# Performance work log

Measured on AMD Instinct MI355X. Metric: run time of the kernel, lower is better.

The kernel has to match this reference:

```python
import jax, jax.numpy as jnp
import numpy as np
from jax import lax

B, C, H = 16384, 512, 1024
IN = C + 4  # context + prev_delta(2) + heading(2)
LN_EPS = 1e-5


def _layernorm(x, g, b):
    mu = x.mean(-1, keepdims=True)
    var = ((x - mu) ** 2).mean(-1, keepdims=True)
    return (x - mu) * lax.rsqrt(var + LN_EPS) * g + b


def setup_inputs() -> dict:
    key = jax.random.key(0)
    ks = jax.random.split(key, 16)
    s = lambda fan_in: 1.0 / np.sqrt(fan_in)
    return {
        "context": jax.random.normal(ks[0], (B, C), jnp.float32),
        "last_pos": jax.random.normal(ks[1], (B, 2), jnp.float32),
        "last_delta": jax.random.normal(ks[2], (B, 2), jnp.float32) * 0.1,
        "Wh": jax.random.normal(ks[3], (H, C), jnp.float32) * s(C),
        "bh": jnp.zeros((H,), jnp.float32),
        "Wc": jax.random.normal(ks[4], (H, C), jnp.float32) * s(C),
        "bc": jnp.zeros((H,), jnp.float32),
        "W_ih": jax.random.normal(ks[5], (4 * H, IN), jnp.float32) * s(H),
        "b_ih": jax.random.normal(ks[6], (4 * H,), jnp.float32) * s(H),
        "W_hh": jax.random.normal(ks[7], (4 * H, H), jnp.float32) * s(H),
        "b_hh": jax.random.normal(ks[8], (4 * H,), jnp.float32) * s(H),
        "ln_g": jnp.ones((H,), jnp.float32),
        "ln_b": jnp.zeros((H,), jnp.float32),
        "W1": jax.random.normal(ks[9], (H, H), jnp.float32) * s(H),
        "b1": jnp.zeros((H,), jnp.float32),
        "W2": jax.random.normal(ks[10], (2, H), jnp.float32) * s(H),
        "b2": jnp.zeros((2,), jnp.float32),
        "pred_len": 60,
    }


def reference(context, last_pos, last_delta, Wh, bh, Wc, bc, W_ih, b_ih, W_hh, b_hh,
              ln_g, ln_b, W1, b1, W2, b2, pred_len):
    hidden = jnp.tanh(context @ Wh.T + bh)
    cell = jnp.tanh(context @ Wc.T + bc)
    # context part of LSTM input gates is constant across steps: precompute
    gates_ctx = context @ W_ih[:, :C].T + b_ih  # [B, 4H]
    W_extra = W_ih[:, C:]  # [4H, 4]

    def step(carry, _):
        h, c, pos, pd = carry
        heading = pd / jnp.maximum(jnp.linalg.norm(pd, axis=-1, keepdims=True), 1e-6)
        extra = jnp.concatenate([pd, heading], axis=-1)  # [B,4]
        gates = gates_ctx + extra @ W_extra.T + h @ W_hh.T + b_hh
        i, f, g, o = jnp.split(gates, 4, axis=-1)
        c = jax.nn.sigmoid(f) * c + jax.nn.sigmoid(i) * jnp.tanh(g)
        h = jax.nn.sigmoid(o) * jnp.tanh(c)
        y = _layernorm(h, ln_g, ln_b)  # dropout is identity in eval
        y = jax.nn.gelu(y @ W1.T + b1, approximate=False)
        delta = y @ W2.T + b2  # [B,2]
        pos = pos + delta
        return (h, c, pos, delta), pos

    _, outs = lax.scan(step, (hidden, cell, last_pos, last_delta), None, length=pred_len)
    return jnp.swapaxes(outs, 0, 1)  # [B, pred_len, 2]
```

## Files before the change

### kernel.cpp

```cpp
#include <hip/hip_runtime.h>
#include <math.h>

constexpr int BATCH = 16384;
constexpr int CDIM  = 512;
constexpr int HDIM  = 1024;
constexpr int GDIM  = 4096;
constexpr int TSTEP = 60;
constexpr float LOSC  = 2048.0f;
constexpr float ILOSC = 1.0f / 2048.0f;

typedef _Float16 half_t;
typedef _Float16 halfx8 __attribute__((ext_vector_type(8)));
typedef _Float16 halfx4 __attribute__((ext_vector_type(4)));
typedef float    f32x4  __attribute__((ext_vector_type(4)));
typedef int      i32x4  __attribute__((ext_vector_type(4)));
typedef signed char i8_t;

__device__ __forceinline__ void async_cp16(const void* g, void* l) {
  __builtin_amdgcn_global_load_lds((__attribute__((address_space(1))) void*)g,
                                   (__attribute__((address_space(3))) void*)l,
                                   16, 0, 0);
}

__device__ __forceinline__ half_t hi16(float x) { return (half_t)x; }
__device__ __forceinline__ half_t lo16(float x) {
  return (half_t)((x - (float)((half_t)x)) * LOSC);
}
__device__ __forceinline__ int clamp8(int v) {
  return v > 127 ? 127 : (v < -127 ? -127 : v);
}
__device__ __forceinline__ float sigf(float x) { return 1.0f / (1.0f + expf(-x)); }
__device__ __forceinline__ float geluf(float v) {
  return 0.5f * v * (1.0f + erff(v * 0.70710678118f));
}

__device__ __forceinline__ void swizzle_tiles(int& mt, int& nt) {
  const int gx = gridDim.x, gy = gridDim.y;
  if (gy & 7) { mt = blockIdx.x; nt = blockIdx.y; return; }
  const int lin = blockIdx.y * gx + blockIdx.x;
  const int xcd = lin & 7;
  const int slot = lin >> 3;
  const int npx = gy >> 3;
  nt = xcd * npx + (slot % npx);
  mt = slot / npx;
}

__device__ __forceinline__ void kstep(f32x4 (&acc)[4][4],
    const half_t* __restrict__ A, size_t lda, int krel,
    const half_t* __restrict__ W, size_t ldw, int kw,
    half_t* sA, half_t* sB, int bm0, int bn0) {
  const int tid  = threadIdx.x;
  const int lane = tid & 63;
  const int wave = tid >> 6;
  const int wm = wave >> 1, wn = wave & 1;
  const int ar = lane >> 2;
  const int ak = (lane & 3) * 8;
  const int quad = lane >> 4;
  const int lcol = lane & 15;
#pragma unroll
  for (int cc = 0; cc < 2; ++cc) {
    const int chunk = wave + cc * 4;
    async_cp16(A + (size_t)(bm0 + chunk * 16 + ar) * lda + (krel + ak), sA + chunk * 512);
    async_cp16(W + (size_t)(bn0 + chunk * 16 + ar) * ldw + (kw + ak), sB + chunk * 512);
  }
  asm volatile("s_waitcnt vmcnt(0)" ::: "memory");
  __syncthreads();
  halfx8 af[4], bfr[4];
#pragma unroll
  for (int mi = 0; mi < 4; ++mi)
    af[mi] = *(const halfx8*)&sA[(wm * 64 + mi * 16 + lcol) * 32 + quad * 8];
#pragma unroll
  for (int ni = 0; ni < 4; ++ni)
    bfr[ni] = *(const halfx8*)&sB[(wn * 64 + ni * 16 + lcol) * 32 + quad * 8];
#pragma unroll
  for (int mi = 0; mi < 4; ++mi)
#pragma unroll
    for (int ni = 0; ni < 4; ++ni)
      acc[mi][ni] = __builtin_amdgcn_mfma_f32_16x16x32_f16(af[mi], bfr[ni], acc[mi][ni], 0, 0, 0);
  __syncthreads();
}

__device__ __forceinline__ void scale_acc4(f32x4 (&acc)[4][4], float s) {
#pragma unroll
  for (int i = 0; i < 4; ++i)
#pragma unroll
    for (int j = 0; j < 4; ++j) acc[i][j] *= s;
}

template <int ACT, bool SPLITOUT>
__global__ __launch_bounds__(256, 3)
void gemm3_pre(const half_t* __restrict__ Ahi, const half_t* __restrict__ Alo,
               const half_t* __restrict__ Wcat, const float* __restrict__ bias,
               float* __restrict__ Cf, half_t* __restrict__ Chi,
               i8_t* __restrict__ C8, int ldc) {
  __shared__ __align__(16) half_t sA[128 * 32];
  __shared__ __align__(16) half_t sB[128 * 32];
  const int tid = threadIdx.x;
  int mt, nt;
  swizzle_tiles(mt, nt);
  const int bm0 = mt * 128, bn0 = nt * 128;
  f32x4 acc[4][4];
#pragma unroll
  for (int i = 0; i < 4; ++i)
#pragma unroll
    for (int j = 0; j < 4; ++j) acc[i][j] = (f32x4){0.f, 0.f, 0.f, 0.f};
#pragma unroll 1
  for (int k0 = 0; k0 < 512; k0 += 32)
    kstep(acc, Ahi, CDIM, k0, Wcat, 1536, k0, sA, sB, bm0, bn0);
#pragma unroll 1
  for (int k0 = 512; k0 < 1024; k0 += 32)
    kstep(acc, Alo, CDIM, k0 - 512, Wcat, 1536, k0, sA, sB, bm0, bn0);
  scale_acc4(acc, ILOSC);
#pragma unroll 1
  for (int k0 = 1024; k0 < 1536; k0 += 32)
    kstep(acc, Ahi, CDIM, k0 - 1024, Wcat, 1536, k0, sA, sB, bm0, bn0);

  const int lane = tid & 63, wave = tid >> 6;
  const int wm = wave >> 1, wn = wave & 1, quad = lane >> 4, lcol = lane & 15;
#pragma unroll
  for (int ni = 0; ni < 4; ++ni) {
    const int col = bn0 + wn * 64 + ni * 16 + lcol;
    const float bv = bias[col];
#pragma unroll
    for (int mi = 0; mi < 4; ++mi) {
      const int row0 = bm0 + wm * 64 + mi * 16 + quad * 4;
#pragma unroll
      for (int r = 0; r < 4; ++r) {
        float v = acc[mi][ni][r] + bv;
        if (ACT == 1) v = tanhf(v);
        if (SPLITOUT) {
          const half_t hh = hi16(v);
          const float hiF = (float)hh;
          Chi[(size_t)(row0 + r) * ldc + col] = hh;
          const int hq = clamp8((int)rintf(hiF * 128.0f));
          const int lq = clamp8((int)rintf((v - hiF) * 524288.0f));
          C8[(size_t)(row0 + r) * 2048 + col]        = (i8_t)hq;
          C8[(size_t)(row0 + r) * 2048 + 1024 + col] = (i8_t)lq;
        } else {
          Cf[(size_t)(row0 + r) * ldc + col] = v;
        }
      }
    }
  }
}

__global__ __launch_bounds__(256, 3)
void gemm_gates_cell(const half_t* __restrict__ hAhi, const i8_t* __restrict__ hA8,
                     const half_t* __restrict__ Whh16, const i8_t* __restrict__ Whh8,
                     const int* __restrict__ Ebuf,
                     const float* __restrict__ gctx,
                     const float* __restrict__ dprev, const float* __restrict__ b2,
                     const float* __restrict__ Wxt, float* __restrict__ c,
                     half_t* __restrict__ hBhi, i8_t* __restrict__ hB8,
                     float* __restrict__ statsT) {
  __shared__ __align__(16) unsigned char sAraw[8192];
  __shared__ __align__(16) unsigned char sBraw[8192];
  __shared__ __align__(16) float sE[4][16 * 68];
  const int tid = threadIdx.x;
  const int lane = tid & 63;
  const int wave = tid >> 6;
  const int wm = wave >> 1, wn = wave & 1;
  const int quad = lane >> 4;
  const int lcol = lane & 15;
  int mt, nt;
  swizzle_tiles(mt, nt);
  const int bm0 = mt * 128, bn0 = nt * 128;

  i32x4 acc8[4][4];
#pragma unroll
  for (int i = 0; i < 4; ++i)
#pragma unroll
    for (int j = 0; j < 4; ++j) acc8[i][j] = (i32x4){0, 0, 0, 0};
  {
    const int ar8 = lane >> 2;
    const int ab8 = (lane & 3) * 16;
#pragma unroll 1
    for (int k0 = 0; k0 < 2048; k0 += 64) {
#pragma unroll
      for (int cc = 0; cc < 2; ++cc) {
        const int chunk = wave + cc * 4;
        async_cp16(hA8 + (size_t)(bm0 + chunk * 16 + ar8) * 2048 + (k0 + ab8),
                   sAraw + chunk * 1024);
        async_cp16(Whh8 + (size_t)(bn0 + chunk * 16 + ar8) * 2048 + (k0 + ab8),
                   sBraw + chunk * 1024);
      }
      asm volatile("s_waitcnt vmcnt(0)" ::: "memory");
      __syncthreads();
      i32x4 ai[4], bi[4];
#pragma unroll
      for (int mi = 0; mi < 4; ++mi)
        ai[mi] = *(const i32x4*)&sAraw[(wm * 64 + mi * 16 + lcol) * 64 + quad * 16];
#pragma unroll
      for (int ni = 0; ni < 4; ++ni)
        bi[ni] = *(const i32x4*)&sBraw[(wn * 64 + ni * 16 + lcol) * 64 + quad * 16];
#pragma unroll
      for (int mi = 0; mi < 4; ++mi)
#pragma unroll
        for (int ni = 0; ni < 4; ++ni)
          acc8[mi][ni] = __builtin_amdgcn_mfma_i32_16x16x64_i8(ai[mi], bi[ni], acc8[mi][ni], 0, 0, 0);
      __syncthreads();
    }
  }
  const int E = Ebuf[0];
  f32x4 acc[4][4];
#pragma unroll
  for (int i = 0; i < 4; ++i)
#pragma unroll
    for (int j = 0; j < 4; ++j)
#pragma unroll
      for (int r = 0; r < 4; ++r)
        acc[i][j][r] = ldexpf((float)acc8[i][j][r], E - 25);

#pragma unroll 1
  for (int k0 = 0; k0 < 1024; k0 += 32)
    kstep(acc, hAhi, HDIM, k0, Whh16, 1024, k0,
          (half_t*)sAraw, (half_t*)sBraw, bm0, bn0);

  float* myE = sE[wave];
  const int u = lane & 15;
  const int q = lane >> 4;
  const int j = ((bn0 + wn * 64) >> 2) + u;
  const float b20 = b2[0], b21 = b2[1];
  const float4 wx0 = *(const float4*)(Wxt + (size_t)j * 16 + 0);
  const float4 wx1 = *(const float4*)(Wxt + (size_t)j * 16 + 4);
  const float4 wx2 = *(const float4*)(Wxt + (size_t)j * 16 + 8);
  const float4 wx3 = *(const float4*)(Wxt + (size_t)j * 16 + 12);

#pragma unroll
  for (int mi = 0; mi < 4; ++mi) {
#pragma unroll
    for (int ni = 0; ni < 4; ++ni)
#pragma unroll
      for (int r = 0; r < 4; ++r)
        myE[(quad * 4 + r) * 68 + ni * 16 + lcol] = acc[mi][ni][r];
#pragma unroll
    for (int k = 0; k < 4; ++k) {
      const int rr = q + 4 * k;
      const int row = bm0 + wm * 64 + mi * 16 + rr;
      const f32x4 gv = *(const f32x4*)&myE[rr * 68 + u * 4];
      const float4 gc = *(const float4*)(gctx + (size_t)row * GDIM + 4 * j);
      const float dx = dprev[2 * row] + b20;
      const float dy = dprev[2 * row + 1] + b21;
      const float nrm = fmaxf(sqrtf(dx * dx + dy * dy), 1e-6f);
      const float ex = dx, ey = dy, ehx = dx / nrm, ehy = dy / nrm;
      const float pi = gv[0] + gc.x + ex*wx0.x + ey*wx0.y + ehx*wx0.z + ehy*wx0.w;
      const float pf = gv[1] + gc.y + ex*wx1.x + ey*wx1.y + ehx*wx1.z + ehy*wx1.w;
      const float pg = gv[2] + gc.z + ex*wx2.x + ey*wx2.y + ehx*wx2.z + ehy*wx2.w;
      const float po = gv[3] + gc.w + ex*wx3.x + ey*wx3.y + ehx*wx3.z + ehy*wx3.w;
      const size_t cidx = (size_t)row * HDIM + j;
      const float cn = sigf(pf) * c[cidx] + sigf(pi) * tanhf(pg);
      c[cidx] = cn;
      const float vh = sigf(po) * tanhf(cn);
      const half_t hh = hi16(vh);
      const float hiF = (float)hh;
      hBhi[cidx] = hh;
      const int hq = clamp8((int)rintf(hiF * 128.0f));
      const int lq = clamp8((int)rintf((vh - hiF) * 524288.0f));
      hB8[(size_t)row * 2048 + j]        = (i8_t)hq;
      hB8[(size_t)row * 2048 + 1024 + j] = (i8_t)lq;
      float ps = vh, pq = vh * vh;
#pragma unroll
      for (int m = 1; m < 16; m <<= 1) {
        ps += __shfl_xor(ps, m, 64);
        pq += __shfl_xor(pq, m, 64);
      }
      if (u == 0) {
        atomicAdd(&statsT[2 * row], ps);
        atomicAdd(&statsT[2 * row + 1], pq);
      }
    }
  }
}

__global__ __launch_bounds__(256, 3)
void gemm_mlp64(const half_t* __restrict__ hBhi, const i8_t* __restrict__ hB8,
                const half_t* __restrict__ W1hi, const i8_t* __restrict__ W18,
                const int* __restrict__ Ebuf, const float* __restrict__ statsT,
                const float* __restrict__ v1, const float* __restrict__ v2,
                const float* __restrict__ W2, float* __restrict__ deltaT) {
  __shared__ __align__(16) unsigned char sAraw[8192];
  __shared__ __align__(16) unsigned char sBraw[4096];
  const int tid = threadIdx.x;
  const int lane = tid & 63;
  const int wave = tid >> 6;
  const int quad = lane >> 4;
  const int lcol = lane & 15;
  int mt, nt;
  swizzle_tiles(mt, nt);
  const int bm0 = mt * 128, bn0 = nt * 64;

  i32x4 acc8[2][4];
#pragma unroll
  for (int i = 0; i < 2; ++i)
#pragma unroll
    for (int jj = 0; jj < 4; ++jj) acc8[i][jj] = (i32x4){0, 0, 0, 0};
  {
    const int ar8 = lane >> 2;
    const int ab8 = (lane & 3) * 16;
#pragma unroll 1
    for (int k0 = 0; k0 < 2048; k0 += 64) {
#pragma unroll
      for (int cc = 0; cc < 2; ++cc) {
        const int chunk = wave + cc * 4;
        async_cp16(hB8 + (size_t)(bm0 + chunk * 16 + ar8) * 2048 + (k0 + ab8),
                   sAraw + chunk * 1024);
      }
      async_cp16(W18 + (size_t)(bn0 + wave * 16 + ar8) * 2048 + (k0 + ab8),
                 sBraw + wave * 1024);
      asm volatile("s_waitcnt vmcnt(0)" ::: "memory");
      __syncthreads();
      i32x4 ai[2], bi[4];
#pragma unroll
      for (int mi = 0; mi < 2; ++mi)
        ai[mi] = *(const i32x4*)&sAraw[(wave * 32 + mi * 16 + lcol) * 64 + quad * 16];
#pragma unroll
      for (int ni = 0; ni < 4; ++ni)
        bi[ni] = *(const i32x4*)&sBraw[(ni * 16 + lcol) * 64 + quad * 16];
#pragma unroll
      for (int mi = 0; mi < 2; ++mi)
#pragma unroll
        for (int ni = 0; ni < 4; ++ni)
          acc8[mi][ni] = __builtin_amdgcn_mfma_i32_16x16x64_i8(ai[mi], bi[ni], acc8[mi][ni], 0, 0, 0);
      __syncthreads();
    }
  }
  const int E1 = Ebuf[1];
  f32x4 accM[2][4];
#pragma unroll
  for (int i = 0; i < 2; ++i)
#pragma unroll
    for (int jj = 0; jj < 4; ++jj)
#pragma unroll
      for (int r = 0; r < 4; ++r)
        accM[i][jj][r] = ldexpf((float)acc8[i][jj][r], E1 - 25);

  {
    half_t* sA = (half_t*)sAraw;
    half_t* sB = (half_t*)sBraw;
    const int ar = lane >> 2;
    const int ak = (lane & 3) * 8;
#pragma unroll 1
    for (int k0 = 0; k0 < 1024; k0 += 32) {
#pragma unroll
      for (int cc = 0; cc < 2; ++cc) {
        const int chunk = wave + cc * 4;
        async_cp16(hBhi + (size_t)(bm0 + chunk * 16 + ar) * HDIM + (k0 + ak), sA + chunk * 512);
      }
      async_cp16(W1hi + (size_t)(bn0 + wave * 16 + ar) * HDIM + (k0 + ak), sB + wave * 512);
      asm volatile("s_waitcnt vmcnt(0)" ::: "memory");
      __syncthreads();
      halfx8 af[2], bfr[4];
#pragma unroll
      for (int mi = 0; mi < 2; ++mi)
        af[mi] = *(const halfx8*)&sA[(wave * 32 + mi * 16 + lcol) * 32 + quad * 8];
#pragma unroll
      for (int ni = 0; ni < 4; ++ni)
        bfr[ni] = *(const halfx8*)&sB[(ni * 16 + lcol) * 32 + quad * 8];
#pragma unroll
      for (int mi = 0; mi < 2; ++mi)
#pragma unroll
        for (int ni = 0; ni < 4; ++ni)
          accM[mi][ni] = __builtin_amdgcn_mfma_f32_16x16x32_f16(af[mi], bfr[ni], accM[mi][ni], 0, 0, 0);
      __syncthreads();
    }
  }

  float w2a[4], w2b[4], v1c[4], v2c[4];
#pragma unroll
  for (int ni = 0; ni < 4; ++ni) {
    const int col = bn0 + ni * 16 + lcol;
    w2a[ni] = W2[col]; w2b[ni] = W2[HDIM + col];
    v1c[ni] = v1[col]; v2c[ni] = v2[col];
  }
#pragma unroll
  for (int mi = 0; mi < 2; ++mi) {
#pragma unroll
    for (int r = 0; r < 4; ++r) {
      const int row = bm0 + wave * 32 + mi * 16 + quad * 4 + r;
      const float S = statsT[2 * row], Q = statsT[2 * row + 1];
      const float mu = S * (1.0f / HDIM);
      const float rs = rsqrtf(Q * (1.0f / HDIM) - mu * mu + 1e-5f);
      float d0 = 0.f, d1 = 0.f;
#pragma unroll
      for (int ni = 0; ni < 4; ++ni) {
        const float g = geluf(rs * (accM[mi][ni][r] - mu * v1c[ni]) + v2c[ni]);
        d0 += g * w2a[ni];
        d1 += g * w2b[ni];
      }
#pragma unroll
      for (int m = 1; m < 16; m <<= 1) {
        d0 += __shfl_xor(d0, m, 64);
        d1 += __shfl_xor(d1, m, 64);
      }
      if (lcol == 0) {
        atomicAdd(&deltaT[2 * row], d0);
        atomicAdd(&deltaT[2 * row + 1], d1);
      }
    }
  }
}

__global__ __launch_bounds__(256)
void write_traj(const float* __restrict__ lp, const float* __restrict__ deltaT,
                const float* __restrict__ b2, float* __restrict__ out, int M) {
  const int b = blockIdx.x * 256 + threadIdx.x;
  if (b >= M) return;
  float px = lp[2 * b], py = lp[2 * b + 1];
  const float b20 = b2[0], b21 = b2[1];
  for (int t = 0; t < TSTEP; ++t) {
    px += deltaT[(size_t)t * M * 2 + 2 * b] + b20;
    py += deltaT[(size_t)t * M * 2 + 2 * b + 1] + b21;
    out[((size_t)b * TSTEP + t) * 2 + 0] = px;
    out[((size_t)b * TSTEP + t) * 2 + 1] = py;
  }
}

__global__ __launch_bounds__(256)
void cvt_split(const float* __restrict__ s, half_t* __restrict__ dhi,
               half_t* __restrict__ dlo, int n4) {
  int i = blockIdx.x * 256 + threadIdx.x;
  if (i >= n4) return;
  const float4 v = ((const float4*)s)[i];
  halfx4 h = { hi16(v.x), hi16(v.y), hi16(v.z), hi16(v.w) };
  halfx4 l = { lo16(v.x), lo16(v.y), lo16(v.z), lo16(v.w) };
  *(halfx4*)(dhi + (size_t)i * 4) = h;
  *(halfx4*)(dlo + (size_t)i * 4) = l;
}

__global__ __launch_bounds__(256)
void wmax_reduce(const float* __restrict__ W, unsigned* __restrict__ mx, int n) {
  float m = 0.f;
  for (int i = blockIdx.x * 256 + threadIdx.x; i < n; i += gridDim.x * 256)
    m = fmaxf(m, fabsf(W[i]));
#pragma unroll
  for (int off = 32; off > 0; off >>= 1)
    m = fmaxf(m, __shfl_down(m, off, 64));
  if ((threadIdx.x & 63) == 0) atomicMax(mx, __float_as_uint(m));
}

__global__ __launch_bounds__(256)
void wmax_w1g(const float* __restrict__ W1, const float* __restrict__ g,
              unsigned* __restrict__ mx) {
  float m = 0.f;
  for (int i = blockIdx.x * 256 + threadIdx.x; i < HDIM * HDIM; i += gridDim.x * 256)
    m = fmaxf(m, fabsf(W1[i] * g[i & 1023]));
#pragma unroll
  for (int off = 32; off > 0; off >>= 1)
    m = fmaxf(m, __shfl_down(m, off, 64));
  if ((threadIdx.x & 63) == 0) atomicMax(mx, __float_as_uint(m));
}

__global__ void set_E(const unsigned* __restrict__ mx, int* __restrict__ Ebuf) {
  int e;
  frexpf(__uint_as_float(mx[0]), &e);
  Ebuf[0] = e - 1;
  frexpf(__uint_as_float(mx[1]), &e);
  Ebuf[1] = e - 1;
}

__global__ __launch_bounds__(256)
void build_whh_hyb(const float* __restrict__ Whh, const int* __restrict__ Ebuf,
                   half_t* __restrict__ W16, i8_t* __restrict__ W8) {
  int idx = blockIdx.x * 256 + threadIdx.x;
  if (idx >= GDIM * HDIM) return;
  const int rp = idx >> 10;
  const int k  = idx & 1023;
  const int sr = (rp & 3) * HDIM + (rp >> 2);
  const float w = Whh[(size_t)sr * HDIM + k];
  const half_t whi = (half_t)w;
  const float hiF = (float)whi;
  const float wlo = w - hiF;
  const int E = Ebuf[0];
  W16[(size_t)rp * 1024 + k] = whi;
  W8[(size_t)rp * 2048 + k]        = (i8_t)clamp8((int)rintf(ldexpf(wlo, 18 - E)));
  W8[(size_t)rp * 2048 + 1024 + k] = (i8_t)clamp8((int)rintf(ldexpf(hiF, 6 - E)));
}

__global__ __launch_bounds__(256)
void build_w1_hyb(const float* __restrict__ W1, const float* __restrict__ g,
                  const float* __restrict__ beta, const float* __restrict__ b1,
                  const int* __restrict__ Ebuf, half_t* __restrict__ W1hi,
                  i8_t* __restrict__ W18, float* __restrict__ v1,
                  float* __restrict__ v2) {
  const int n = blockIdx.x;
  const int tid = threadIdx.x;
  const int k = tid * 4;
  const int E1 = Ebuf[1];
  const float4 w  = *(const float4*)(W1 + (size_t)n * HDIM + k);
  const float4 gg = *(const float4*)(g + k);
  const float4 bb = *(const float4*)(beta + k);
  float wg[4] = { w.x*gg.x, w.y*gg.y, w.z*gg.z, w.w*gg.w };
  halfx4 hh;
  float s1 = 0.f;
#pragma unroll
  for (int u = 0; u < 4; ++u) {
    const half_t h = (half_t)wg[u];
    hh[u] = h;
    const float hiF = (float)h;
    const float lo = wg[u] - hiF;
    W18[(size_t)n * 2048 + k + u]        = (i8_t)clamp8((int)rintf(ldexpf(lo, 18 - E1)));
    W18[(size_t)n * 2048 + 1024 + k + u] = (i8_t)clamp8((int)rintf(ldexpf(hiF, 6 - E1)));
    s1 += wg[u];
  }
  *(halfx4*)(W1hi + (size_t)n * HDIM + k) = hh;
  float s2 = w.x*bb.x + w.y*bb.y + w.z*bb.z + w.w*bb.w;
#pragma unroll
  for (int off = 32; off > 0; off >>= 1) {
    s1 += __shfl_down(s1, off, 64);
    s2 += __shfl_down(s2, off, 64);
  }
  __shared__ float t1[4], t2[4];
  const int wv = tid >> 6, ln = tid & 63;
  if (ln == 0) { t1[wv] = s1; t2[wv] = s2; }
  __syncthreads();
  if (tid == 0) {
    v1[n] = t1[0] + t1[1] + t1[2] + t1[3];
    v2[n] = t2[0] + t2[1] + t2[2] + t2[3] + b1[n];
  }
}

__global__ __launch_bounds__(256)
void build_wx(const float* __restrict__ Wih, float* __restrict__ Wxt) {
  int rp = blockIdx.x * 256 + threadIdx.x;
  if (rp >= GDIM) return;
  const int jj = rp >> 2, g = rp & 3;
  const int sr = g * HDIM + jj;
  const float4 v = *(const float4*)(Wih + (size_t)sr * 516 + 512);
  *(float4*)(Wxt + (size_t)jj * 16 + g * 4) = v;
}

__global__ __launch_bounds__(256)
void build_wih_cat(const float* __restrict__ Wih, half_t* __restrict__ dst) {
  int idx = blockIdx.x * 256 + threadIdx.x;
  if (idx >= GDIM * 384) return;
  const int rp = idx / 384;
  const int k  = (idx - rp * 384) * 4;
  const int sr = (rp & 3) * HDIM + (rp >> 2);
  const bool lo = (k < 512);
  const int kk = lo ? k : (k < 1024 ? k - 512 : k - 1024);
  const float4 v = *(const float4*)(Wih + (size_t)sr * 516 + kk);
  half_t* d = dst + (size_t)rp * 1536 + k;
  if (lo) { halfx4 o = { lo16(v.x), lo16(v.y), lo16(v.z), lo16(v.w) }; *(halfx4*)d = o; }
  else    { halfx4 o = { hi16(v.x), hi16(v.y), hi16(v.z), hi16(v.w) }; *(halfx4*)d = o; }
}

__global__ __launch_bounds__(256)
void build_bias(const float* __restrict__ b_ih, const float* __restrict__ b_hh,
                float* __restrict__ bias_i) {
  int rp = blockIdx.x * 256 + threadIdx.x;
  if (rp >= GDIM) return;
  const int sr = (rp & 3) * HDIM + (rp >> 2);
  bias_i[rp] = b_ih[sr] + b_hh[sr];
}

__global__ __launch_bounds__(128)
void build_wc_cat(const float* __restrict__ W, half_t* __restrict__ dst) {
  const int n = blockIdx.x;
  const int k = threadIdx.x * 4;
  const float4 w = *(const float4*)(W + (size_t)n * CDIM + k);
  halfx4 hl = { lo16(w.x), lo16(w.y), lo16(w.z), lo16(w.w) };
  halfx4 hh = { hi16(w.x), hi16(w.y), hi16(w.z), hi16(w.w) };
  *(halfx4*)(dst + (size_t)n * 1536 + k)        = hl;
  *(halfx4*)(dst + (size_t)n * 1536 + 512 + k)  = hh;
  *(halfx4*)(dst + (size_t)n * 1536 + 1024 + k) = hh;
}

__global__ __launch_bounds__(256)
void init_chunk(const float* __restrict__ ld, const float* __restrict__ b2,
                float* __restrict__ delta_init, int M) {
  int b = blockIdx.x * 256 + threadIdx.x;
  if (b >= M) return;
  delta_init[2*b]   = ld[2*b]   - b2[0];
  delta_init[2*b+1] = ld[2*b+1] - b2[1];
}

extern "C" void kernel_launch(void* const* d_in, const int* in_sizes, int n_in,
                              void* d_out, int out_size, void* d_ws, size_t ws_size,
                              hipStream_t stream) {
  const float* context    = (const float*)d_in[0];
  const float* last_pos   = (const float*)d_in[1];
  const float* last_delta = (const float*)d_in[2];
  const float* Wh   = (const float*)d_in[3];
  const float* bh   = (const float*)d_in[4];
  const float* Wc   = (const float*)d_in[5];
  const float* bc   = (const float*)d_in[6];
  const float* W_ih = (const float*)d_in[7];
  const float* b_ih = (const float*)d_in[8];
  const float* W_hh = (const float*)d_in[9];
  const float* b_hh = (const float*)d_in[10];
  const float* ln_g = (const float*)d_in[11];
  const float* ln_b = (const float*)d_in[12];
  const float* W1   = (const float*)d_in[13];
  const float* b1   = (const float*)d_in[14];
  const float* W2   = (const float*)d_in[15];
  const float* b2   = (const float*)d_in[16];
  float* out = (float*)d_out;

  const size_t stat_bytes =
      (size_t)GDIM * 1024 * 2 +
      (size_t)GDIM * 2048 +
      (size_t)GDIM * 1536 * 2 +
      (size_t)HDIM * 1024 * 2 +
      (size_t)HDIM * 2048 +
      2 * (size_t)HDIM * 1536 * 2 +
      (size_t)HDIM * 16 * 4 + (size_t)GDIM * 4 + 2 * (size_t)HDIM * 4 + 32768;
  int NC = 0;
  for (int nc : {2, 4, 8, 16}) {
    const size_t M = BATCH / nc;
    const size_t chunk_bytes = 2 * M * HDIM * 2 +
                               2 * M * 2048 +
                               2 * M * CDIM * 2 +
                               M * HDIM * 4 +
                               (size_t)M * GDIM * 4 +
                               M * 2 * 4 +
                               2 * (size_t)TSTEP * M * 2 * 4 + 32768;
    if (stat_bytes + chunk_bytes <= ws_size) { NC = nc; break; }
  }
  if (NC == 0) return;
  const int M = BATCH / NC;

  char* w = (char*)d_ws;
  auto take = [&](size_t bytes) {
    char* p = w;
    w += (bytes + 255) & ~(size_t)255;
    return p;
  };
  half_t* Whh16   = (half_t*)take((size_t)GDIM * 1024 * 2);
  i8_t*   Whh8    = (i8_t*)take((size_t)GDIM * 2048);
  half_t* Wih_cat = (half_t*)take((size_t)GDIM * 1536 * 2);
  half_t* W1hi    = (half_t*)take((size_t)HDIM * 1024 * 2);
  i8_t*   W18     = (i8_t*)take((size_t)HDIM * 2048);
  half_t* Wh_cat  = (half_t*)take((size_t)HDIM * 1536 * 2);
  half_t* Wc_cat  = (half_t*)take((size_t)HDIM * 1536 * 2);
  float*  Wxt     = (float*)take((size_t)HDIM * 16 * 4);
  float*  bias_i  = (float*)take((size_t)GDIM * 4);
  float*  v1      = (float*)take((size_t)HDIM * 4);
  float*  v2      = (float*)take((size_t)HDIM * 4);
  unsigned* mx    = (unsigned*)take(256);
  int*    Ebuf    = (int*)take(256);
  half_t* h0hi    = (half_t*)take((size_t)M * HDIM * 2);
  half_t* h1hi    = (half_t*)take((size_t)M * HDIM * 2);
  i8_t*   h08     = (i8_t*)take((size_t)M * 2048);
  i8_t*   h18     = (i8_t*)take((size_t)M * 2048);
  half_t* ctx_hi  = (half_t*)take((size_t)M * CDIM * 2);
  half_t* ctx_lo  = (half_t*)take((size_t)M * CDIM * 2);
  float*  c_f     = (float*)take((size_t)M * HDIM * 4);
  float*  gctx    = (float*)take((size_t)M * GDIM * 4);
  float*  dinit   = (float*)take((size_t)M * 2 * 4);
  const size_t sd_bytes = 2 * (size_t)TSTEP * M * 2 * 4;
  float*  statsAll = (float*)take(sd_bytes);
  float*  deltaAll = statsAll + (size_t)TSTEP * M * 2;

  hipMemsetAsync(mx, 0, 8, stream);
  wmax_reduce<<<256, 256, 0, stream>>>(W_hh, mx, GDIM * HDIM);
  wmax_w1g<<<256, 256, 0, stream>>>(W1, ln_g, mx + 1);
  set_E<<<1, 1, 0, stream>>>(mx, Ebuf);
  build_whh_hyb<<<(GDIM * HDIM + 255) / 256, 256, 0, stream>>>(W_hh, Ebuf, Whh16, Whh8);
  build_w1_hyb<<<HDIM, 256, 0, stream>>>(W1, ln_g, ln_b, b1, Ebuf, W1hi, W18, v1, v2);
  build_wx<<<(GDIM + 255) / 256, 256, 0, stream>>>(W_ih, Wxt);
  build_wih_cat<<<(GDIM * 384 + 255) / 256, 256, 0, stream>>>(W_ih, Wih_cat);
  build_bias<<<(GDIM + 255) / 256, 256, 0, stream>>>(b_ih, b_hh, bias_i);
  build_wc_cat<<<HDIM, 128, 0, stream>>>(Wh, Wh_cat);
  build_wc_cat<<<HDIM, 128, 0, stream>>>(Wc, Wc_cat);

  const dim3 blk(256);
  for (int chunk = 0; chunk < NC; ++chunk) {
    const size_t base = (size_t)chunk * M;
    hipMemsetAsync(statsAll, 0, sd_bytes, stream);
    cvt_split<<<(M * CDIM / 4 + 255) / 256, 256, 0, stream>>>(
        context + base * CDIM, ctx_hi, ctx_lo, M * CDIM / 4);
    gemm3_pre<1, true ><<<dim3(M/128, HDIM/128), blk, 0, stream>>>(
        ctx_hi, ctx_lo, Wh_cat, bh, nullptr, h0hi, h08, HDIM);
    gemm3_pre<1, false><<<dim3(M/128, HDIM/128), blk, 0, stream>>>(
        ctx_hi, ctx_lo, Wc_cat, bc, c_f, nullptr, nullptr, HDIM);
    gemm3_pre<0, false><<<dim3(M/128, GDIM/128), blk, 0, stream>>>(
        ctx_hi, ctx_lo, Wih_cat, bias_i, gctx, nullptr, nullptr, GDIM);
    init_chunk<<<(M + 255) / 256, 256, 0, stream>>>(
        last_delta + base * 2, b2, dinit, M);

    const half_t* hAhi = h0hi;
    const i8_t* hA8 = h08;
    half_t* hBhi = h1hi;
    i8_t* hB8 = h18;
    for (int t = 0; t < TSTEP; ++t) {
      const float* dprev = (t == 0) ? dinit : deltaAll + (size_t)(t - 1) * M * 2;
      gemm_gates_cell<<<dim3(M/128, GDIM/128), blk, 0, stream>>>(
          hAhi, hA8, Whh16, Whh8, Ebuf, gctx, dprev, b2, Wxt, c_f,
          hBhi, hB8, statsAll + (size_t)t * M * 2);
      gemm_mlp64<<<dim3(M/128, HDIM/64), blk, 0, stream>>>(
          hBhi, hB8, W1hi, W18, Ebuf, statsAll + (size_t)t * M * 2, v1, v2, W2,
          deltaAll + (size_t)t * M * 2);
      half_t* th = hBhi; hBhi = (half_t*)hAhi; hAhi = th;
      i8_t* t8 = hB8; hB8 = (i8_t*)hA8; hA8 = t8;
    }
    write_traj<<<(M + 255) / 256, 256, 0, stream>>>(
        last_pos + base * 2, deltaAll, b2, out + base * TSTEP * 2, M);
  }
  (void)in_sizes; (void)n_in; (void)out_size;
}
```

Baseline: 36.32 ms.

## Run batch chunks concurrently on multiple HIP streams with per-stream buffers

Splits the batch into fixed chunks of 2048 (or 1024) rows and spreads them round-robin over up to four streams, each with its own scratch buffers, using events to fork from and join back to the main stream. Chunks advance their 60-step recurrence in parallel, so small per-step GEMM grids from different chunks can share the GPU and hide launch gaps. The cost is more workspace, more L2 pressure since chunks share weights, and streams and events created on every call and never destroyed. Chunk size also changes compared with the old scheme, which picked the largest chunk that fit.

```diff
diff --git a/kernel.cpp b/kernel.cpp
--- a/kernel.cpp
+++ b/kernel.cpp
@@ -597,27 +597,28 @@
   float* out = (float*)d_out;
 
   const size_t stat_bytes =
-      (size_t)GDIM * 1024 * 2 +
-      (size_t)GDIM * 2048 +
-      (size_t)GDIM * 1536 * 2 +
-      (size_t)HDIM * 1024 * 2 +
-      (size_t)HDIM * 2048 +
+      (size_t)GDIM * 1024 * 2 + (size_t)GDIM * 2048 + (size_t)GDIM * 1536 * 2 +
+      (size_t)HDIM * 1024 * 2 + (size_t)HDIM * 2048 +
       2 * (size_t)HDIM * 1536 * 2 +
       (size_t)HDIM * 16 * 4 + (size_t)GDIM * 4 + 2 * (size_t)HDIM * 4 + 32768;
-  int NC = 0;
-  for (int nc : {2, 4, 8, 16}) {
-    const size_t M = BATCH / nc;
-    const size_t chunk_bytes = 2 * M * HDIM * 2 +
-                               2 * M * 2048 +
-                               2 * M * CDIM * 2 +
-                               M * HDIM * 4 +
-                               (size_t)M * GDIM * 4 +
-                               M * 2 * 4 +
-                               2 * (size_t)TSTEP * M * 2 * 4 + 32768;
-    if (stat_bytes + chunk_bytes <= ws_size) { NC = nc; break; }
-  }
-  if (NC == 0) return;
-  const int M = BATCH / NC;
+  auto chain_bytes = [](size_t M) {
+    return 2 * M * HDIM * 2 +
+           2 * M * 2048 +
+           2 * M * CDIM * 2 +
+           M * HDIM * 4 +
+           M * (size_t)GDIM * 4 +
+           M * 2 * 4 +
+           2 * (size_t)TSTEP * M * 2 * 4 + 65536;
+  };
+  int NSTR = 0, M = 0;
+  const int cand[5][2] = { {4, 2048}, {2, 2048}, {2, 1024}, {1, 2048}, {1, 1024} };
+  for (int ci = 0; ci < 5; ++ci) {
+    if (stat_bytes + (size_t)cand[ci][0] * chain_bytes(cand[ci][1]) <= ws_size) {
+      NSTR = cand[ci][0]; M = cand[ci][1]; break;
+    }
+  }
+  if (NSTR == 0) return;
+  const int NCHUNK = BATCH / M;
 
   char* w = (char*)d_ws;
   auto take = [&](size_t bytes) {
@@ -638,18 +639,29 @@
   float*  v2      = (float*)take((size_t)HDIM * 4);
   unsigned* mx    = (unsigned*)take(256);
   int*    Ebuf    = (int*)take(256);
-  half_t* h0hi    = (half_t*)take((size_t)M * HDIM * 2);
-  half_t* h1hi    = (half_t*)take((size_t)M * HDIM * 2);
-  i8_t*   h08     = (i8_t*)take((size_t)M * 2048);
-  i8_t*   h18     = (i8_t*)take((size_t)M * 2048);
-  half_t* ctx_hi  = (half_t*)take((size_t)M * CDIM * 2);
-  half_t* ctx_lo  = (half_t*)take((size_t)M * CDIM * 2);
-  float*  c_f     = (float*)take((size_t)M * HDIM * 4);
-  float*  gctx    = (float*)take((size_t)M * GDIM * 4);
-  float*  dinit   = (float*)take((size_t)M * 2 * 4);
-  const size_t sd_bytes = 2 * (size_t)TSTEP * M * 2 * 4;
-  float*  statsAll = (float*)take(sd_bytes);
-  float*  deltaAll = statsAll + (size_t)TSTEP * M * 2;
+
+  struct ChainBuf {
+    half_t *h0hi, *h1hi;
+    i8_t *h08, *h18;
+    half_t *ctx_hi, *ctx_lo;
+    float *c_f, *gctx, *dinit, *statsAll, *deltaAll;
+    size_t sd_bytes;
+  };
+  ChainBuf cb[4];
+  for (int s = 0; s < NSTR; ++s) {
+    cb[s].h0hi   = (half_t*)take((size_t)M * HDIM * 2);
+    cb[s].h1hi   = (half_t*)take((size_t)M * HDIM * 2);
+    cb[s].h08    = (i8_t*)take((size_t)M * 2048);
+    cb[s].h18    = (i8_t*)take((size_t)M * 2048);
+    cb[s].ctx_hi = (half_t*)take((size_t)M * CDIM * 2);
+    cb[s].ctx_lo = (half_t*)take((size_t)M * CDIM * 2);
+    cb[s].c_f    = (float*)take((size_t)M * HDIM * 4);
+    cb[s].gctx   = (float*)take((size_t)M * GDIM * 4);
+    cb[s].dinit  = (float*)take((size_t)M * 2 * 4);
+    cb[s].sd_bytes = 2 * (size_t)TSTEP * M * 2 * 4;
+    cb[s].statsAll = (float*)take(cb[s].sd_bytes);
+    cb[s].deltaAll = cb[s].statsAll + (size_t)TSTEP * M * 2;
+  }
 
   hipMemsetAsync(mx, 0, 8, stream);
   wmax_reduce<<<256, 256, 0, stream>>>(W_hh, mx, GDIM * HDIM);
@@ -663,38 +675,62 @@
   build_wc_cat<<<HDIM, 128, 0, stream>>>(Wh, Wh_cat);
   build_wc_cat<<<HDIM, 128, 0, stream>>>(Wc, Wc_cat);
 
+  hipStream_t str[4];
+  str[0] = stream;
+  hipEvent_t eFork = nullptr, eJoin[4] = {nullptr, nullptr, nullptr, nullptr};
+  if (NSTR > 1) {
+    hipEventCreateWithFlags(&eFork, hipEventDisableTiming);
+    hipEventRecord(eFork, stream);
+    for (int s = 1; s < NSTR; ++s) {
+      hipStreamCreateWithFlags(&str[s], hipStreamNonBlocking);
+      hipStreamWaitEvent(str[s], eFork, 0);
+      hipEventCreateWithFlags(&eJoin[s], hipEventDisableTiming);
+    }
+  }
+
   const dim3 blk(256);
-  for (int chunk = 0; chunk < NC; ++chunk) {
-    const size_t base = (size_t)chunk * M;
-    hipMemsetAsync(statsAll, 0, sd_bytes, stream);
-    cvt_split<<<(M * CDIM / 4 + 255) / 256, 256, 0, stream>>>(
-        context + base * CDIM, ctx_hi, ctx_lo, M * CDIM / 4);
-    gemm3_pre<1, true ><<<dim3(M/128, HDIM/128), blk, 0, stream>>>(
-        ctx_hi, ctx_lo, Wh_cat, bh, nullptr, h0hi, h08, HDIM);
-    gemm3_pre<1, false><<<dim3(M/128, HDIM/128), blk, 0, stream>>>(
-        ctx_hi, ctx_lo, Wc_cat, bc, c_f, nullptr, nullptr, HDIM);
-    gemm3_pre<0, false><<<dim3(M/128, GDIM/128), blk, 0, stream>>>(
-        ctx_hi, ctx_lo, Wih_cat, bias_i, gctx, nullptr, nullptr, GDIM);
-    init_chunk<<<(M + 255) / 256, 256, 0, stream>>>(
-        last_delta + base * 2, b2, dinit, M);
-
-    const half_t* hAhi = h0hi;
-    const i8_t* hA8 = h08;
-    half_t* hBhi = h1hi;
-    i8_t* hB8 = h18;
+  auto run_chunk = [&](hipStream_t st, ChainBuf& B, size_t base) {
+    hipMemsetAsync(B.statsAll, 0, B.sd_bytes, st);
+    cvt_split<<<(M * CDIM / 4 + 255) / 256, 256, 0, st>>>(
+        context + base * CDIM, B.ctx_hi, B.ctx_lo, M * CDIM / 4);
+    gemm3_pre<1, true ><<<dim3(M/128, HDIM/128), blk, 0, st>>>(
+        B.ctx_hi, B.ctx_lo, Wh_cat, bh, nullptr, B.h0hi, B.h08, HDIM);
+    gemm3_pre<1, false><<<dim3(M/128, HDIM/128), blk, 0, st>>>(
+        B.ctx_hi, B.ctx_lo, Wc_cat, bc, B.c_f, nullptr, nullptr, HDIM);
+    gemm3_pre<0, false><<<dim3(M/128, GDIM/128), blk, 0, st>>>(
+        B.ctx_hi, B.ctx_lo, Wih_cat, bias_i, B.gctx, nullptr, nullptr, GDIM);
+    init_chunk<<<(M + 255) / 256, 256, 0, st>>>(
+        last_delta + base * 2, b2, B.dinit, M);
+
+    const half_t* hAhi = B.h0hi;
+    const i8_t* hA8 = B.h08;
+    half_t* hBhi = B.h1hi;
+    i8_t* hB8 = B.h18;
     for (int t = 0; t < TSTEP; ++t) {
-      const float* dprev = (t == 0) ? dinit : deltaAll + (size_t)(t - 1) * M * 2;
-      gemm_gates_cell<<<dim3(M/128, GDIM/128), blk, 0, stream>>>(
-          hAhi, hA8, Whh16, Whh8, Ebuf, gctx, dprev, b2, Wxt, c_f,
-          hBhi, hB8, statsAll + (size_t)t * M * 2);
-      gemm_mlp64<<<dim3(M/128, HDIM/64), blk, 0, stream>>>(
-          hBhi, hB8, W1hi, W18, Ebuf, statsAll + (size_t)t * M * 2, v1, v2, W2,
-          deltaAll + (size_t)t * M * 2);
+      const float* dprev = (t == 0) ? B.dinit : B.deltaAll + (size_t)(t - 1) * M * 2;
+      gemm_gates_cell<<<dim3(M/128, GDIM/128), blk, 0, st>>>(
+          hAhi, hA8, Whh16, Whh8, Ebuf, B.gctx, dprev, b2, Wxt, B.c_f,
+          hBhi, hB8, B.statsAll + (size_t)t * M * 2);
+      gemm_mlp64<<<dim3(M/128, HDIM/64), blk, 0, st>>>(
+          hBhi, hB8, W1hi, W18, Ebuf, B.statsAll + (size_t)t * M * 2, v1, v2, W2,
+          B.deltaAll + (size_t)t * M * 2);
       half_t* th = hBhi; hBhi = (half_t*)hAhi; hAhi = th;
       i8_t* t8 = hB8; hB8 = (i8_t*)hA8; hA8 = t8;
     }
-    write_traj<<<(M + 255) / 256, 256, 0, stream>>>(
-        last_pos + base * 2, deltaAll, b2, out + base * TSTEP * 2, M);
+    write_traj<<<(M + 255) / 256, 256, 0, st>>>(
+        last_pos + base * 2, B.deltaAll, b2, out + base * TSTEP * 2, M);
+  };
+
+  for (int i = 0; i < NCHUNK; ++i) {
+    const int s = i % NSTR;
+    run_chunk(str[s], cb[s], (size_t)i * M);
+  }
+
+  if (NSTR > 1) {
+    for (int s = 1; s < NSTR; ++s) {
+      hipEventRecord(eJoin[s], str[s]);
+      hipStreamWaitEvent(stream, eJoin[s], 0);
+    }
   }
   (void)in_sizes; (void)n_in; (void)out_size;
 }
```

After: 35.79 ms. Within noise of the previous version (-1.5%).
